# Performance work log

Measured on AMD Instinct MI355X. Metric: run time of the kernel, lower is better.

## Reference

```python
import jax, jax.numpy as jnp
import numpy as np

B, N, F, HID, N_I, N_O = 4096, 128, 28, 512, 4, 4
G = N_I + N_O
SELF = 36
TAU = 1.0


def setup_inputs() -> dict:
    key = jax.random.key(0)
    ks = jax.random.split(key, 7)
    s = lambda k, shp, fan: jax.random.normal(k, shp, jnp.float32) * (1.0 / np.sqrt(fan))
    return {
        "x": jax.random.normal(ks[0], (B, SELF + N * F), jnp.float32),
        "W1": s(ks[1], (F, HID), F),
        "b1": jnp.zeros((HID,), jnp.float32),
        "W2": s(ks[2], (HID, G), HID),
        "b2": jnp.zeros((G,), jnp.float32),
        "Wa": s(ks[3], (SELF + N_I * N * F + N_O * F, HID), SELF + N_I * N * F + N_O * F),
        "ba": jnp.zeros((HID,), jnp.float32),
    }


def reference(x, W1, b1, W2, b2, Wa, ba):
    batch = x.shape[0]
    self_info = x[:, :SELF]                      # [B, 36]
    o = x[:, SELF:].reshape(batch, N, F)         # [B, N, 28] (== split(28)+stack+permute)

    # gating MLP -> group logits [B, N, G]
    h = jnp.maximum(jnp.einsum("bnf,fh->bnh", o, W1) + b1, 0.0)
    logits = jnp.einsum("bnh,hg->bng", h, W2) + b2

    # gumbel-softmax, hard=True (straight-through), fixed noise key
    g = jax.random.gumbel(jax.random.key(42), logits.shape, jnp.float32)
    y_soft = jax.nn.softmax((logits + g) / TAU, axis=2)
    hard = jax.nn.one_hot(jnp.argmax(y_soft, axis=2), G, dtype=y_soft.dtype)
    y = jax.lax.stop_gradient(hard - y_soft) + y_soft

    mask = jnp.transpose(y, (0, 2, 1))           # [B, G, N]
    igroup_mask = mask[:, :N_I]                  # [B, n1, N]
    ogroup_mask = mask[:, N_I:]                  # [B, n2, N]

    # aggregate other groups: bmm -> [B, n2, 28]
    ogroup_em = jnp.einsum("bgn,bnf->bgf", ogroup_mask, o)
    # important groups: hadamard broadcast -> [B, n1, N, 28]
    igroup_em = igroup_mask[:, :, :, None] * o[:, None, :, :]

    em = jnp.concatenate(
        [self_info, igroup_em.reshape(batch, -1), ogroup_em.reshape(batch, -1)], axis=1
    )
    out = em @ Wa + ba                           # [B, HID]
    return out, igroup_mask, ogroup_mask
```

## Files before the change

### kernel.cpp

```cpp
#include <hip/hip_runtime.h>
#include <hip/hip_bf16.h>

#define BB 4096
#define NN 128
#define FF 28
#define HH 512
#define GG 8
#define NI 4
#define SELFW 36
#define XROW 3620
#define IG_BASE 36
#define OG_BASE 14372

typedef short v8s __attribute__((ext_vector_type(8)));
typedef float v16f __attribute__((ext_vector_type(16)));
typedef unsigned v4u __attribute__((ext_vector_type(4)));

__device__ __forceinline__ unsigned rotl32(unsigned x, unsigned r) {
    return (x << r) | (x >> (32u - r));
}

__device__ __forceinline__ unsigned threefry_bits(unsigned idx) {
    unsigned x0 = 0u, x1 = idx;
    const unsigned k0 = 0u, k1 = 42u, k2 = 0x1BD11BDAu ^ 0u ^ 42u;
    x0 += k0; x1 += k1;
#define R4(a,b,c,d) \
    x0 += x1; x1 = rotl32(x1,(a)); x1 ^= x0; \
    x0 += x1; x1 = rotl32(x1,(b)); x1 ^= x0; \
    x0 += x1; x1 = rotl32(x1,(c)); x1 ^= x0; \
    x0 += x1; x1 = rotl32(x1,(d)); x1 ^= x0;
    R4(13,15,26,6)   x0 += k1; x1 += k2 + 1u;
    R4(17,29,16,24)  x0 += k2; x1 += k0 + 2u;
    R4(13,15,26,6)   x0 += k0; x1 += k1 + 3u;
    R4(17,29,16,24)  x0 += k1; x1 += k2 + 4u;
    R4(13,15,26,6)   x0 += k2; x1 += k0 + 5u;
#undef R4
    return x0 ^ x1;
}

__device__ __forceinline__ float gumbel_at(unsigned idx) {
    unsigned bits = threefry_bits(idx);
    float f = __uint_as_float((bits >> 9) | 0x3f800000u) - 1.0f;
    float u = fmaxf(f, 1.17549435e-38f);
    return -logf(-logf(u));
}

__device__ __forceinline__ unsigned pk2(float a, float b) {
    __hip_bfloat162 h = __float22bfloat162_rn(make_float2(a, b));
    union { __hip_bfloat162 h; unsigned u; } c; c.h = h; return c.u;
}

__device__ __forceinline__ v8s as8s(v4u v) {
    union { v4u u; v8s s; } c; c.u = v; return c.s;
}

__global__ __launch_bounds__(256) void k_prep(
    const float* __restrict__ Wa, unsigned short* __restrict__ Wbt)
{
    int tid = blockIdx.x * 256 + threadIdx.x;
    int h = tid & 511, gn = tid >> 9;
    const float* src = Wa + (size_t)(IG_BASE + gn * FF) * HH + h;
    unsigned w[16];
#pragma unroll
    for (int q = 0; q < 14; ++q) w[q] = pk2(src[(2*q) * HH], src[(2*q+1) * HH]);
    w[14] = 0u; w[15] = 0u;
    v4u* dst = (v4u*)(Wbt + (size_t)tid * 32);
    dst[0] = v4u{w[0],  w[1],  w[2],  w[3]};
    dst[1] = v4u{w[4],  w[5],  w[6],  w[7]};
    dst[2] = v4u{w[8],  w[9],  w[10], w[11]};
    dst[3] = v4u{w[12], w[13], w[14], w[15]};
}

__global__ __launch_bounds__(256, 2) void k_route(
    const float* __restrict__ x, const float* __restrict__ W1,
    const float* __restrict__ b1, const float* __restrict__ W2,
    const float* __restrict__ b2,
    unsigned char* __restrict__ grp, unsigned char* __restrict__ grpT,
    float* __restrict__ ig_mask, float* __restrict__ og_mask)
{
    __shared__ float w1t[HH * FF];
    __shared__ float w2s[HH * GG];
    __shared__ float b1s[HH];

    for (int i = threadIdx.x; i < FF * HH; i += 256) {
        int f = i / HH, j = i % HH;
        w1t[j * FF + f] = W1[i];
    }
    for (int i = threadIdx.x; i < HH * GG; i += 256) w2s[i] = W2[i];
    for (int i = threadIdx.x; i < HH; i += 256) b1s[i] = b1[i];
    __syncthreads();

    float b2r[GG];
#pragma unroll
    for (int g = 0; g < GG; ++g) b2r[g] = b2[g];

    int tid = blockIdx.x * 256 + threadIdx.x;
    int nthreads = gridDim.x * 256;
    for (int item = tid; item < BB * NN; item += nthreads) {
        int b = item >> 7, n = item & 127;
        const float4* op = (const float4*)(x + (size_t)b * XROW + SELFW + n * FF);
        float o[FF];
#pragma unroll
        for (int q = 0; q < 7; ++q) {
            float4 v = op[q];
            o[4*q+0] = v.x; o[4*q+1] = v.y; o[4*q+2] = v.z; o[4*q+3] = v.w;
        }
        float acc[GG];
#pragma unroll
        for (int g = 0; g < GG; ++g) acc[g] = 0.0f;

        for (int j = 0; j < HH; ++j) {
            const float4* wr = (const float4*)(w1t + j * FF);
            float h = 0.0f;
#pragma unroll
            for (int q = 0; q < 7; ++q) {
                float4 w = wr[q];
                h = fmaf(o[4*q+0], w.x, h);
                h = fmaf(o[4*q+1], w.y, h);
                h = fmaf(o[4*q+2], w.z, h);
                h = fmaf(o[4*q+3], w.w, h);
            }
            h += b1s[j];
            h = fmaxf(h, 0.0f);
            const float4* w2r = (const float4*)(w2s + j * GG);
            float4 wa = w2r[0], wb = w2r[1];
            acc[0] = fmaf(h, wa.x, acc[0]);
            acc[1] = fmaf(h, wa.y, acc[1]);
            acc[2] = fmaf(h, wa.z, acc[2]);
            acc[3] = fmaf(h, wa.w, acc[3]);
            acc[4] = fmaf(h, wb.x, acc[4]);
            acc[5] = fmaf(h, wb.y, acc[5]);
            acc[6] = fmaf(h, wb.z, acc[6]);
            acc[7] = fmaf(h, wb.w, acc[7]);
        }

        int best = 0;
        float bz = acc[0] + b2r[0] + gumbel_at(((unsigned)item << 3) + 0u);
#pragma unroll
        for (int g = 1; g < GG; ++g) {
            float z = acc[g] + b2r[g] + gumbel_at(((unsigned)item << 3) + (unsigned)g);
            if (z > bz) { bz = z; best = g; }
        }

        grp[item] = (unsigned char)best;
        grpT[(size_t)n * BB + b] = (unsigned char)best;
        if (best < NI) ig_mask[(size_t)b * 512 + best * 128 + n] = 1.0f;
        else           og_mask[(size_t)b * 512 + (best - NI) * 128 + n] = 1.0f;
    }
}

__global__ __launch_bounds__(256) void k_ogem(
    const float* __restrict__ x, const unsigned char* __restrict__ grp,
    float* __restrict__ og_em)
{
    int t = threadIdx.x;
    int bl = t >> 5, f = t & 31;
    size_t b = (size_t)blockIdx.x * 8 + bl;
    if (f >= FF) return;
    const unsigned char* gp = grp + b * NN;
    const float* xp = x + b * XROW + SELFW;
    float a0 = 0.f, a1 = 0.f, a2 = 0.f, a3 = 0.f;
    for (int n = 0; n < NN; ++n) {
        int g = gp[n];
        float v = xp[n * FF + f];
        a0 += (g == 4) ? v : 0.0f;
        a1 += (g == 5) ? v : 0.0f;
        a2 += (g == 6) ? v : 0.0f;
        a3 += (g == 7) ? v : 0.0f;
    }
    float* e = og_em + b * 112 + f;
    e[0] = a0; e[28] = a1; e[56] = a2; e[84] = a3;
}

__global__ __launch_bounds__(256) void k_dense(
    const float* __restrict__ x, const float* __restrict__ og_em,
    const float* __restrict__ Wa, const float* __restrict__ ba,
    float* __restrict__ out)
{
    __shared__ float As[16][148];
    int t = threadIdx.x;
    size_t b0 = (size_t)blockIdx.x * 16;
    for (int i = t; i < 16 * 148; i += 256) {
        int bl = i / 148, k = i % 148;
        As[bl][k] = (k < SELFW) ? x[(b0 + bl) * XROW + k]
                                : og_em[(b0 + bl) * 112 + (k - SELFW)];
    }
    __syncthreads();
    int lane = t & 63, wv = t >> 6;
    int h0 = lane * 8;
    float acc[4][8];
#pragma unroll
    for (int i = 0; i < 4; ++i)
#pragma unroll
        for (int j = 0; j < 8; ++j) acc[i][j] = 0.0f;

    for (int k = 0; k < 148; ++k) {
        int row = (k < SELFW) ? k : (OG_BASE + k - SELFW);
        const float4* wr = (const float4*)(Wa + (size_t)row * HH + h0);
        float4 wA = wr[0], wB = wr[1];
#pragma unroll
        for (int i = 0; i < 4; ++i) {
            float a = As[wv * 4 + i][k];
            acc[i][0] = fmaf(a, wA.x, acc[i][0]);
            acc[i][1] = fmaf(a, wA.y, acc[i][1]);
            acc[i][2] = fmaf(a, wA.z, acc[i][2]);
            acc[i][3] = fmaf(a, wA.w, acc[i][3]);
            acc[i][4] = fmaf(a, wB.x, acc[i][4]);
            acc[i][5] = fmaf(a, wB.y, acc[i][5]);
            acc[i][6] = fmaf(a, wB.z, acc[i][6]);
            acc[i][7] = fmaf(a, wB.w, acc[i][7]);
        }
    }
    float4 baA = *(const float4*)(ba + h0);
    float4 baB = *(const float4*)(ba + h0 + 4);
    float bav[8] = {baA.x, baA.y, baA.z, baA.w, baB.x, baB.y, baB.z, baB.w};
#pragma unroll
    for (int i = 0; i < 4; ++i) {
        float* opt = out + (b0 + wv * 4 + i) * HH + h0;
#pragma unroll
        for (int j = 0; j < 8; ++j) opt[j] = acc[i][j] + bav[j];
    }
}

__global__ __launch_bounds__(128) void k_ig(
    const float* __restrict__ x, const unsigned char* __restrict__ grpT,
    const unsigned short* __restrict__ Wbt, float* __restrict__ out)
{
    __shared__ v4u A4[2][256];
    __shared__ v4u B4[2][1024];
    __shared__ unsigned Gs_u[2048];

    int t = threadIdx.x;
    int b0 = (blockIdx.x >> 3) * 64;
    int h0 = (blockIdx.x & 7) * 64;
    int lane = t & 63;
    int wn = t >> 6;
    int l31 = lane & 31, lhi = lane >> 5;

    const unsigned* gTu = (const unsigned*)grpT;
#pragma unroll
    for (int j = 0; j < 16; ++j) {
        int i = t + j * 128;
        Gs_u[i] = gTu[(size_t)(i >> 4) * (BB/4) + (b0 >> 2) + (i & 15)];
    }

    v16f acc0 = {}, acc1 = {};

    int s_row = t >> 1, s_fh = t & 1;
    int s_sw = (s_row >> 1) & 3;
#define STAGE(nn, buf) do {                                                     \
    const float* s = x + (size_t)(b0 + s_row) * XROW + SELFW + (nn) * FF + s_fh * 16; \
    float4 fA = *(const float4*)(s + 0);                                        \
    float4 fB = *(const float4*)(s + 4);                                        \
    float4 fC = *(const float4*)(s + 8);                                        \
    float4 fD = s_fh ? make_float4(0.f,0.f,0.f,0.f) : *(const float4*)(s + 12); \
    v4u w0 = v4u{pk2(fA.x,fA.y), pk2(fA.z,fA.w), pk2(fB.x,fB.y), pk2(fB.z,fB.w)}; \
    v4u w1 = v4u{pk2(fC.x,fC.y), pk2(fC.z,fC.w), pk2(fD.x,fD.y), pk2(fD.z,fD.w)}; \
    A4[buf][s_row * 4 + ((s_fh * 2    ) ^ s_sw)] = w0;                          \
    A4[buf][s_row * 4 + ((s_fh * 2 + 1) ^ s_sw)] = w1;                          \
    _Pragma("unroll")                                                           \
    for (int j = 0; j < 8; ++j) {                                               \
        int i = t + j * 128;                                                    \
        int fg = i & 3, hh = (i >> 2) & 63, e = i >> 8;                         \
        v4u v = ((const v4u*)Wbt)[((size_t)(e * 128 + (nn)) * HH + h0 + hh) * 4 + fg]; \
        B4[buf][(e * 64 + hh) * 4 + (fg ^ ((hh >> 1) & 3))] = v;                \
    }                                                                           \
} while (0)

    STAGE(0, 0);
    int cur = 0;
    int r0 = l31, r1 = 32 + l31;
    int sw0 = (r0 >> 1) & 3, sw1 = (r1 >> 1) & 3;
    int hl = wn * 32 + l31;
    int swh = (hl >> 1) & 3;

    for (int n = 0; n < NN; ++n) {
        __syncthreads();
        unsigned char g0r = ((const unsigned char*)Gs_u)[n * 64 + r0];
        unsigned char g1r = ((const unsigned char*)Gs_u)[n * 64 + r1];
        v4u a00 = A4[cur][r0 * 4 + ((lhi    ) ^ sw0)];
        v4u a01 = A4[cur][r0 * 4 + ((2 + lhi) ^ sw0)];
        v4u a10 = A4[cur][r1 * 4 + ((lhi    ) ^ sw1)];
        v4u a11 = A4[cur][r1 * 4 + ((2 + lhi) ^ sw1)];
        v4u bf[4][2];
#pragma unroll
        for (int e = 0; e < 4; ++e) {
            bf[e][0] = B4[cur][(e * 64 + hl) * 4 + ((lhi    ) ^ swh)];
            bf[e][1] = B4[cur][(e * 64 + hl) * 4 + ((2 + lhi) ^ swh)];
        }
        if (n + 1 < NN) STAGE(n + 1, cur ^ 1);
        v4u zz = {0u, 0u, 0u, 0u};
#pragma unroll
        for (int e = 0; e < 4; ++e) {
            v4u m00 = (g0r == e) ? a00 : zz;
            v4u m01 = (g0r == e) ? a01 : zz;
            v4u m10 = (g1r == e) ? a10 : zz;
            v4u m11 = (g1r == e) ? a11 : zz;
            acc0 = __builtin_amdgcn_mfma_f32_32x32x16_bf16(as8s(m00), as8s(bf[e][0]), acc0, 0, 0, 0);
            acc0 = __builtin_amdgcn_mfma_f32_32x32x16_bf16(as8s(m01), as8s(bf[e][1]), acc0, 0, 0, 0);
            acc1 = __builtin_amdgcn_mfma_f32_32x32x16_bf16(as8s(m10), as8s(bf[e][0]), acc1, 0, 0, 0);
            acc1 = __builtin_amdgcn_mfma_f32_32x32x16_bf16(as8s(m11), as8s(bf[e][1]), acc1, 0, 0, 0);
        }
        cur ^= 1;
    }
#undef STAGE

#pragma unroll
    for (int r = 0; r < 16; ++r) {
        int rowl = (r & 3) + 8 * (r >> 2) + 4 * lhi;
        size_t i0 = (size_t)(b0 + rowl) * HH + h0 + wn * 32 + l31;
        out[i0] += acc0[r];
        out[i0 + (size_t)32 * HH] += acc1[r];
    }
}

extern "C" void kernel_launch(void* const* d_in, const int* in_sizes, int n_in,
                              void* d_out, int out_size, void* d_ws, size_t ws_size,
                              hipStream_t stream)
{
    const float* x  = (const float*)d_in[0];
    const float* W1 = (const float*)d_in[1];
    const float* b1 = (const float*)d_in[2];
    const float* W2 = (const float*)d_in[3];
    const float* b2 = (const float*)d_in[4];
    const float* Wa = (const float*)d_in[5];
    const float* ba = (const float*)d_in[6];

    float* out     = (float*)d_out;
    float* ig_mask = out + (size_t)BB * HH;
    float* og_mask = ig_mask + (size_t)BB * NI * NN;

    unsigned char* grp  = (unsigned char*)d_ws;
    unsigned char* grpT = grp + (size_t)BB * NN;
    float* og_em = (float*)(grpT + (size_t)BB * NN);
    unsigned short* Wbt = (unsigned short*)((char*)d_ws + 2883584);

    hipMemsetAsync(ig_mask, 0, (size_t)2 * BB * NI * NN * sizeof(float), stream);

    k_prep <<<1024, 256, 0, stream>>>(Wa, Wbt);
    k_route<<<512, 256, 0, stream>>>(x, W1, b1, W2, b2, grp, grpT, ig_mask, og_mask);
    k_ogem <<<512, 256, 0, stream>>>(x, grp, og_em);
    k_dense<<<256, 256, 0, stream>>>(x, og_em, Wa, ba, out);
    k_ig   <<<512, 128, 0, stream>>>(x, grpT, Wbt, out);
}
```

Baseline: 702.0 us.

## Read routing MLP weights via scalar loads from a pre-transposed global buffer

A small prep kernel writes W1 transposed into 32-float rows, with b1 stored in slot 28. The routing kernel drops its shared-memory staging and uses readfirstlane so the weight addresses are wave-uniform, which lets the compiler turn them into scalar (SMEM) loads broadcast to the whole wave. Removing the large LDS footprint allows more waves per CU, so the grid grows from 512 to 2048 blocks. The risk is that scalar cache bandwidth or latency becomes the bottleneck of the inner loop, and there is one extra kernel launch.

```diff
diff --git a/kernel.cpp b/kernel.cpp
--- a/kernel.cpp
+++ b/kernel.cpp
@@ -71,25 +71,24 @@
     dst[3] = v4u{w[12], w[13], w[14], w[15]};
 }
 
-__global__ __launch_bounds__(256, 2) void k_route(
-    const float* __restrict__ x, const float* __restrict__ W1,
-    const float* __restrict__ b1, const float* __restrict__ W2,
-    const float* __restrict__ b2,
+__global__ __launch_bounds__(256) void k_prep_w1(
+    const float* __restrict__ W1, const float* __restrict__ b1,
+    float* __restrict__ W1T32)
+{
+    int i = blockIdx.x * 256 + threadIdx.x;
+    int j = i & 511, f = i >> 9;
+    float v = 0.0f;
+    if (f < FF) v = W1[f * HH + j];
+    else if (f == FF) v = b1[j];
+    W1T32[j * 32 + f] = v;
+}
+
+__global__ __launch_bounds__(256) void k_route(
+    const float* __restrict__ x, const float* __restrict__ W1T32,
+    const float* __restrict__ W2, const float* __restrict__ b2,
     unsigned char* __restrict__ grp, unsigned char* __restrict__ grpT,
     float* __restrict__ ig_mask, float* __restrict__ og_mask)
 {
-    __shared__ float w1t[HH * FF];
-    __shared__ float w2s[HH * GG];
-    __shared__ float b1s[HH];
-
-    for (int i = threadIdx.x; i < FF * HH; i += 256) {
-        int f = i / HH, j = i % HH;
-        w1t[j * FF + f] = W1[i];
-    }
-    for (int i = threadIdx.x; i < HH * GG; i += 256) w2s[i] = W2[i];
-    for (int i = threadIdx.x; i < HH; i += 256) b1s[i] = b1[i];
-    __syncthreads();
-
     float b2r[GG];
 #pragma unroll
     for (int g = 0; g < GG; ++g) b2r[g] = b2[g];
@@ -110,28 +109,16 @@
         for (int g = 0; g < GG; ++g) acc[g] = 0.0f;
 
         for (int j = 0; j < HH; ++j) {
-            const float4* wr = (const float4*)(w1t + j * FF);
+            int jo = __builtin_amdgcn_readfirstlane(j);
+            const float* wr  = W1T32 + jo * 32;
+            const float* w2r = W2 + jo * GG;
             float h = 0.0f;
 #pragma unroll
-            for (int q = 0; q < 7; ++q) {
-                float4 w = wr[q];
-                h = fmaf(o[4*q+0], w.x, h);
-                h = fmaf(o[4*q+1], w.y, h);
-                h = fmaf(o[4*q+2], w.z, h);
-                h = fmaf(o[4*q+3], w.w, h);
-            }
-            h += b1s[j];
+            for (int f = 0; f < FF; ++f) h = fmaf(o[f], wr[f], h);
+            h += wr[28];
             h = fmaxf(h, 0.0f);
-            const float4* w2r = (const float4*)(w2s + j * GG);
-            float4 wa = w2r[0], wb = w2r[1];
-            acc[0] = fmaf(h, wa.x, acc[0]);
-            acc[1] = fmaf(h, wa.y, acc[1]);
-            acc[2] = fmaf(h, wa.z, acc[2]);
-            acc[3] = fmaf(h, wa.w, acc[3]);
-            acc[4] = fmaf(h, wb.x, acc[4]);
-            acc[5] = fmaf(h, wb.y, acc[5]);
-            acc[6] = fmaf(h, wb.z, acc[6]);
-            acc[7] = fmaf(h, wb.w, acc[7]);
+#pragma unroll
+            for (int g = 0; g < GG; ++g) acc[g] = fmaf(h, w2r[g], acc[g]);
         }
 
         int best = 0;
@@ -334,12 +321,14 @@
     unsigned char* grpT = grp + (size_t)BB * NN;
     float* og_em = (float*)(grpT + (size_t)BB * NN);
     unsigned short* Wbt = (unsigned short*)((char*)d_ws + 2883584);
+    float* W1T32 = (float*)((char*)d_ws + 19660800);
 
     hipMemsetAsync(ig_mask, 0, (size_t)2 * BB * NI * NN * sizeof(float), stream);
 
-    k_prep <<<1024, 256, 0, stream>>>(Wa, Wbt);
-    k_route<<<512, 256, 0, stream>>>(x, W1, b1, W2, b2, grp, grpT, ig_mask, og_mask);
-    k_ogem <<<512, 256, 0, stream>>>(x, grp, og_em);
-    k_dense<<<256, 256, 0, stream>>>(x, og_em, Wa, ba, out);
-    k_ig   <<<512, 128, 0, stream>>>(x, grpT, Wbt, out);
-}
+    k_prep   <<<1024, 256, 0, stream>>>(Wa, Wbt);
+    k_prep_w1<<<64, 256, 0, stream>>>(W1, b1, W1T32);
+    k_route  <<<2048, 256, 0, stream>>>(x, W1T32, W2, b2, grp, grpT, ig_mask, og_mask);
+    k_ogem   <<<512, 256, 0, stream>>>(x, grp, og_em);
+    k_dense  <<<256, 256, 0, stream>>>(x, og_em, Wa, ba, out);
+    k_ig     <<<512, 128, 0, stream>>>(x, grpT, Wbt, out);
+}
```

Result: slower. 718.2 us (+2.3%).
